# Kernel tuning notes

Measured on AMD Instinct MI355X. Metric: run time of the kernel, lower is better.

The kernel has to match this reference:

```python
import jax, jax.numpy as jnp
import numpy as np

SOFTCAP = 30.0
N_CHUNKS = 9
IGNORE_INDEX = -100


def setup_inputs() -> dict:
    key = jax.random.key(0)
    k1, k2, k3 = jax.random.split(key, 3)
    N, D, V = 576, 1024, 262400
    x = jax.random.normal(k1, (N, D), dtype=jnp.float32)
    weight = jax.random.normal(k2, (V, D), dtype=jnp.float32) * (D ** -0.5)
    labels = jax.random.randint(k3, (N,), 0, V, dtype=jnp.int64)
    return {"x": x, "weight": weight, "labels": labels}


def reference(x, weight, labels):
    """Chunked large-vocab softmax cross-entropy with tanh logit soft-capping.

    logits = SOFTCAP * tanh(x @ W.T / SOFTCAP)
    loss   = mean over valid tokens of (logsumexp(logits) - logits[label])
    Chunked over N (9 chunks) so the full [N, V] logits tensor is never
    materialized at once (mirrors the original chunked implementation).
    """
    N, D = x.shape
    chunk = N // N_CHUNKS  # N chosen divisible by N_CHUNKS
    xs = x.reshape(N_CHUNKS, chunk, D)
    ys = labels.reshape(N_CHUNKS, chunk)

    def chunk_nll_sum(xc, yc):
        # [chunk, V] logits for this chunk only
        z = SOFTCAP * jnp.tanh((xc @ weight.T) / SOFTCAP)
        lse = jax.nn.logsumexp(z, axis=-1)                       # [chunk]
        tgt = jnp.take_along_axis(z, jnp.maximum(yc, 0)[:, None], axis=1)[:, 0]
        nll = jnp.where(yc != IGNORE_INDEX, lse - tgt, 0.0)
        return jnp.sum(nll)

    def body(carry, xy):
        xc, yc = xy
        return carry + chunk_nll_sum(xc, yc), None

    total, _ = jax.lax.scan(body, jnp.float32(0.0), (xs, ys))
    n_valid = jnp.sum(labels != IGNORE_INDEX).astype(jnp.float32)
    return total / n_valid
```

## Files before the change

### kernel.cpp

```cpp
#include <hip/hip_runtime.h>
#include <hip/hip_bf16.h>

#define N_TOK   576
#define MPAD    640
#define DIM     1024
#define VOCAB   262400
#define BM      128
#define BN      128
#define BK      64
#define RB      5
#define VBLKS   (VOCAB/BN)
#define NWG     (RB*VBLKS)
#define IGNORE_INDEX (-100)

typedef float f32x4 __attribute__((ext_vector_type(4)));

#define AS1 __attribute__((address_space(1)))
#define AS3 __attribute__((address_space(3)))

__device__ __forceinline__ int cvt4_fp8(float4 v) {
  int r = __builtin_amdgcn_cvt_pk_fp8_f32(v.x, v.y, 0, false);
  r     = __builtin_amdgcn_cvt_pk_fp8_f32(v.z, v.w, r, true);
  return r;
}

__global__ void k_cvt_x(const float* __restrict__ x, unsigned char* __restrict__ xq) {
  int idx = blockIdx.x * 256 + threadIdx.x;
  long e0 = (long)idx * 8;
  int row = (int)(e0 >> 10);
  uint2 o;
  if (row < N_TOK) {
    float4 a = *(const float4*)(x + e0);
    float4 b = *(const float4*)(x + e0 + 4);
    o.x = (unsigned)cvt4_fp8(a);
    o.y = (unsigned)cvt4_fp8(b);
  } else { o.x = o.y = 0u; }
  *(uint2*)(xq + e0) = o;
}

__global__ __launch_bounds__(256, 4) void k_gemm(
    const float* __restrict__ W,
    const unsigned char* __restrict__ Xq,
    float* __restrict__ S)
{
  __shared__ unsigned char Asl[BM * BK];
  __shared__ unsigned char Bsl[BN * BK];

  const int q  = NWG / 8, rm = NWG % 8;
  const int orig = blockIdx.x;
  const int xcd  = orig & 7;
  const int part = orig >> 3;
  const int bid  = (xcd < rm ? xcd * (q + 1) : rm * (q + 1) + (xcd - rm) * q) + part;

  const int rb  = bid % RB;
  const int vb  = bid / RB;
  const int m0  = rb * BM;
  const long n0 = (long)vb * BN;

  const int t   = threadIdx.x;
  const int l   = t & 63;
  const int w   = t >> 6;
  const int wm  = w >> 1, wn = w & 1;
  const int l15 = l & 15, lh = l >> 4;

  const unsigned char* asrc[2];
  #pragma unroll
  for (int i = 0; i < 2; ++i) {
    int lin = t + i * 256;
    int p   = lin >> 3;
    int c   = (lin & 7) ^ (p & 7);
    asrc[i] = Xq + (size_t)(m0 + 2 * p + (c >> 2)) * DIM + (c & 3) * 16;
  }
  const float* bsrc[4];
  int boff[4];
  #pragma unroll
  for (int i = 0; i < 4; ++i) {
    int lin = t + i * 256;
    int r   = lin >> 3;
    int ko  = (lin & 7) * 8;
    bsrc[i] = W + (n0 + r) * DIM + ko;
    int p = r >> 1, s = r & 1;
    int jj = (lin & 7) >> 1, hb = lin & 1;
    boff[i] = p * 128 + ((((s << 2) | jj) ^ (p & 7)) << 4) + (hb << 3);
  }
  const int pr = l15 >> 1, sr = l15 & 1;
  int fo[2];
  #pragma unroll
  for (int kk = 0; kk < 2; ++kk)
    fo[kk] = pr * 128 + (((((sr << 2) | (kk * 2 + (lh >> 1))) ^ pr)) << 4)
           + ((lh & 1) << 3);
  const int abase = wm * 4096;
  const int bbase = wn * 4096;

  f32x4 acc[4][4];
  const f32x4 zero4 = {0.0f, 0.0f, 0.0f, 0.0f};
  #pragma unroll
  for (int i = 0; i < 4; ++i)
    #pragma unroll
    for (int j = 0; j < 4; ++j) acc[i][j] = zero4;

  for (int k0 = 0; k0 < DIM; k0 += BK) {
    float4 fb[4][2];
    #pragma unroll
    for (int i = 0; i < 4; ++i) {
      fb[i][0] = *(const float4*)(bsrc[i] + k0);
      fb[i][1] = *(const float4*)(bsrc[i] + k0 + 4);
    }
    __syncthreads();
    #pragma unroll
    for (int i = 0; i < 2; ++i)
      __builtin_amdgcn_global_load_lds((const AS1 void*)(asrc[i] + k0),
          (AS3 void*)(Asl + (t + i * 256) * 16), 16, 0, 0);
    #pragma unroll
    for (int i = 0; i < 4; ++i) {
      int lo = cvt4_fp8(fb[i][0]);
      int hi = cvt4_fp8(fb[i][1]);
      *(int2*)(Bsl + boff[i]) = make_int2(lo, hi);
    }
    __syncthreads();

    long af[4][2], bf[4][2];
    #pragma unroll
    for (int mi = 0; mi < 4; ++mi) {
      af[mi][0] = *(const long*)(Asl + abase + mi * 1024 + fo[0]);
      af[mi][1] = *(const long*)(Asl + abase + mi * 1024 + fo[1]);
    }
    #pragma unroll
    for (int ni = 0; ni < 4; ++ni) {
      bf[ni][0] = *(const long*)(Bsl + bbase + ni * 1024 + fo[0]);
      bf[ni][1] = *(const long*)(Bsl + bbase + ni * 1024 + fo[1]);
    }
    __builtin_amdgcn_s_setprio(1);
    #pragma unroll
    for (int kk = 0; kk < 2; ++kk)
      #pragma unroll
      for (int mi = 0; mi < 4; ++mi)
        #pragma unroll
        for (int ni = 0; ni < 4; ++ni)
          acc[mi][ni] = __builtin_amdgcn_mfma_f32_16x16x32_fp8_fp8(
              af[mi][kk], bf[ni][kk], acc[mi][ni], 0, 0, 0);
    __builtin_amdgcn_s_setprio(0);
  }

  #pragma unroll
  for (int mi = 0; mi < 4; ++mi) {
    #pragma unroll
    for (int j = 0; j < 4; ++j) {
      float s = 0.0f;
      #pragma unroll
      for (int ni = 0; ni < 4; ++ni) {
        float g   = acc[mi][ni][j];
        float tp1 = __expf(g * (1.0f / 15.0f)) + 1.0f;
        s += __expf(-60.0f * __builtin_amdgcn_rcpf(tp1));
      }
      s += __shfl_xor(s, 1);
      s += __shfl_xor(s, 2);
      s += __shfl_xor(s, 4);
      s += __shfl_xor(s, 8);
      if (l15 == 0) {
        int row = m0 + wm * 64 + mi * 16 + lh * 4 + j;
        atomicAdd(&S[row], s);
      }
    }
  }
}

__global__ void k_tgt(const float* __restrict__ x, const float* __restrict__ W,
                      const int* __restrict__ labels, float* __restrict__ tgt) {
  int n = blockIdx.x;
  int lab = labels[n];
  int t = threadIdx.x;
  float s = 0.0f;
  if (lab >= 0) {
    const float4 a = ((const float4*)(x + (size_t)n * DIM))[t];
    const float4 b = ((const float4*)(W + (size_t)lab * DIM))[t];
    s = a.x*b.x + a.y*b.y + a.z*b.z + a.w*b.w;
  }
  #pragma unroll
  for (int off = 32; off >= 1; off >>= 1) s += __shfl_xor(s, off);
  __shared__ float wsum[4];
  if ((t & 63) == 0) wsum[t >> 6] = s;
  __syncthreads();
  if (t == 0) {
    float d = wsum[0] + wsum[1] + wsum[2] + wsum[3];
    tgt[n] = (lab >= 0) ? 30.0f * tanhf(d * (1.0f / 30.0f)) : 0.0f;
  }
}

__global__ void k_final(const float* __restrict__ S, const float* __restrict__ tgt,
                        const int* __restrict__ labels, float* __restrict__ out) {
  int t = threadIdx.x;
  float sum = 0.0f, cnt = 0.0f;
  for (int n = t; n < N_TOK; n += 256) {
    if (labels[n] != IGNORE_INDEX) {
      sum += 30.0f + __logf(S[n]) - tgt[n];
      cnt += 1.0f;
    }
  }
  #pragma unroll
  for (int off = 32; off >= 1; off >>= 1) {
    sum += __shfl_xor(sum, off);
    cnt += __shfl_xor(cnt, off);
  }
  __shared__ float as_[4], ac_[4];
  if ((t & 63) == 0) { as_[t >> 6] = sum; ac_[t >> 6] = cnt; }
  __syncthreads();
  if (t == 0) out[0] = (as_[0]+as_[1]+as_[2]+as_[3]) / (ac_[0]+ac_[1]+ac_[2]+ac_[3]);
}

extern "C" void kernel_launch(void* const* d_in, const int* in_sizes, int n_in,
                              void* d_out, int out_size, void* d_ws, size_t ws_size,
                              hipStream_t stream) {
  const float* x      = (const float*)d_in[0];
  const float* W      = (const float*)d_in[1];
  const int*   labels = (const int*)d_in[2];
  float* out = (float*)d_out;

  char* ws = (char*)d_ws;
  unsigned char* xq = (unsigned char*)ws;
  float* S   = (float*)(ws + (size_t)MPAD * DIM);
  float* tgt = S + MPAD;

  hipMemsetAsync(S, 0, MPAD * sizeof(float), stream);
  k_cvt_x<<<MPAD * DIM / (256 * 8), 256, 0, stream>>>(x, xq);
  k_gemm<<<NWG, 256, 0, stream>>>(W, xq, S);
  k_tgt<<<N_TOK, 256, 0, stream>>>(x, W, labels, tgt);
  k_final<<<1, 256, 0, stream>>>(S, tgt, labels, out);
}
```

Baseline: 484.4 us.

## Load X fragments directly to registers and use 16-byte LDS reads for W

Removes the LDS staging buffer for the quantized X tile, so each wave loads its own X fragments from global memory straight into registers. It changes the k-slot assignment so each lane holds 16 contiguous bytes, which lets the W tile be read from LDS with one 16-byte load per fragment instead of two 8-byte loads. Barriers now wait only on LDS counters, which lets the global loads overlap the barrier. In exchange the X data is loaded redundantly across waves (the two waves that share wm both fetch it), register pressure rises, and launch bounds drop from 4 to 3 waves per SIMD.

```diff
diff --git a/kernel.cpp b/kernel.cpp
--- a/kernel.cpp
+++ b/kernel.cpp
@@ -15,14 +15,22 @@
 
 typedef float f32x4 __attribute__((ext_vector_type(4)));
 
-#define AS1 __attribute__((address_space(1)))
-#define AS3 __attribute__((address_space(3)))
-
 __device__ __forceinline__ int cvt4_fp8(float4 v) {
   int r = __builtin_amdgcn_cvt_pk_fp8_f32(v.x, v.y, 0, false);
   r     = __builtin_amdgcn_cvt_pk_fp8_f32(v.z, v.w, r, true);
   return r;
 }
+__device__ __forceinline__ long lo64(uint4 v) {
+  union { uint2 u; long l; } c; c.u = make_uint2(v.x, v.y); return c.l;
+}
+__device__ __forceinline__ long hi64(uint4 v) {
+  union { uint2 u; long l; } c; c.u = make_uint2(v.z, v.w); return c.l;
+}
+
+#define BARRIER() do {                                          \
+    asm volatile("s_waitcnt lgkmcnt(0)" ::: "memory");          \
+    __builtin_amdgcn_s_barrier();                               \
+  } while (0)
 
 __global__ void k_cvt_x(const float* __restrict__ x, unsigned char* __restrict__ xq) {
   int idx = blockIdx.x * 256 + threadIdx.x;
@@ -38,12 +46,11 @@
   *(uint2*)(xq + e0) = o;
 }
 
-__global__ __launch_bounds__(256, 4) void k_gemm(
+__global__ __launch_bounds__(256, 3) void k_gemm(
     const float* __restrict__ W,
     const unsigned char* __restrict__ Xq,
     float* __restrict__ S)
 {
-  __shared__ unsigned char Asl[BM * BK];
   __shared__ unsigned char Bsl[BN * BK];
 
   const int q  = NWG / 8, rm = NWG % 8;
@@ -63,34 +70,30 @@
   const int wm  = w >> 1, wn = w & 1;
   const int l15 = l & 15, lh = l >> 4;
 
-  const unsigned char* asrc[2];
-  #pragma unroll
-  for (int i = 0; i < 2; ++i) {
-    int lin = t + i * 256;
-    int p   = lin >> 3;
-    int c   = (lin & 7) ^ (p & 7);
-    asrc[i] = Xq + (size_t)(m0 + 2 * p + (c >> 2)) * DIM + (c & 3) * 16;
-  }
+  const unsigned char* asrc[4];
+  #pragma unroll
+  for (int mi = 0; mi < 4; ++mi)
+    asrc[mi] = Xq + (size_t)(m0 + wm * 64 + mi * 16 + l15) * DIM + lh * 16;
+
   const float* bsrc[4];
   int boff[4];
   #pragma unroll
   for (int i = 0; i < 4; ++i) {
     int lin = t + i * 256;
     int r   = lin >> 3;
-    int ko  = (lin & 7) * 8;
-    bsrc[i] = W + (n0 + r) * DIM + ko;
+    int g   = lin & 7;
+    bsrc[i] = W + (n0 + r) * DIM + g * 8;
     int p = r >> 1, s = r & 1;
-    int jj = (lin & 7) >> 1, hb = lin & 1;
+    int jj = g >> 1, hb = g & 1;
     boff[i] = p * 128 + ((((s << 2) | jj) ^ (p & 7)) << 4) + (hb << 3);
   }
-  const int pr = l15 >> 1, sr = l15 & 1;
-  int fo[2];
-  #pragma unroll
-  for (int kk = 0; kk < 2; ++kk)
-    fo[kk] = pr * 128 + (((((sr << 2) | (kk * 2 + (lh >> 1))) ^ pr)) << 4)
-           + ((lh & 1) << 3);
-  const int abase = wm * 4096;
-  const int bbase = wn * 4096;
+  int bro[4];
+  #pragma unroll
+  for (int ni = 0; ni < 4; ++ni) {
+    int row = wn * 64 + ni * 16 + l15;
+    int p   = row >> 1;
+    bro[ni] = p * 128 + (((((row & 1) << 2) | lh) ^ (p & 7)) << 4);
+  }
 
   f32x4 acc[4][4];
   const f32x4 zero4 = {0.0f, 0.0f, 0.0f, 0.0f};
@@ -106,39 +109,39 @@
       fb[i][0] = *(const float4*)(bsrc[i] + k0);
       fb[i][1] = *(const float4*)(bsrc[i] + k0 + 4);
     }
-    __syncthreads();
-    #pragma unroll
-    for (int i = 0; i < 2; ++i)
-      __builtin_amdgcn_global_load_lds((const AS1 void*)(asrc[i] + k0),
-          (AS3 void*)(Asl + (t + i * 256) * 16), 16, 0, 0);
+    uint4 ua[4];
+    #pragma unroll
+    for (int mi = 0; mi < 4; ++mi)
+      ua[mi] = *(const uint4*)(asrc[mi] + k0);
+
+    BARRIER();
+
     #pragma unroll
     for (int i = 0; i < 4; ++i) {
       int lo = cvt4_fp8(fb[i][0]);
       int hi = cvt4_fp8(fb[i][1]);
       *(int2*)(Bsl + boff[i]) = make_int2(lo, hi);
     }
-    __syncthreads();
-
-    long af[4][2], bf[4][2];
-    #pragma unroll
-    for (int mi = 0; mi < 4; ++mi) {
-      af[mi][0] = *(const long*)(Asl + abase + mi * 1024 + fo[0]);
-      af[mi][1] = *(const long*)(Asl + abase + mi * 1024 + fo[1]);
-    }
-    #pragma unroll
-    for (int ni = 0; ni < 4; ++ni) {
-      bf[ni][0] = *(const long*)(Bsl + bbase + ni * 1024 + fo[0]);
-      bf[ni][1] = *(const long*)(Bsl + bbase + ni * 1024 + fo[1]);
-    }
+    BARRIER();
+
+    uint4 ub[4];
+    #pragma unroll
+    for (int ni = 0; ni < 4; ++ni)
+      ub[ni] = *(const uint4*)(Bsl + bro[ni]);
+
     __builtin_amdgcn_s_setprio(1);
     #pragma unroll
-    for (int kk = 0; kk < 2; ++kk)
+    for (int mi = 0; mi < 4; ++mi)
       #pragma unroll
-      for (int mi = 0; mi < 4; ++mi)
-        #pragma unroll
-        for (int ni = 0; ni < 4; ++ni)
-          acc[mi][ni] = __builtin_amdgcn_mfma_f32_16x16x32_fp8_fp8(
-              af[mi][kk], bf[ni][kk], acc[mi][ni], 0, 0, 0);
+      for (int ni = 0; ni < 4; ++ni)
+        acc[mi][ni] = __builtin_amdgcn_mfma_f32_16x16x32_fp8_fp8(
+            lo64(ua[mi]), lo64(ub[ni]), acc[mi][ni], 0, 0, 0);
+    #pragma unroll
+    for (int mi = 0; mi < 4; ++mi)
+      #pragma unroll
+      for (int ni = 0; ni < 4; ++ni)
+        acc[mi][ni] = __builtin_amdgcn_mfma_f32_16x16x32_fp8_fp8(
+            hi64(ua[mi]), hi64(ub[ni]), acc[mi][ni], 0, 0, 0);
     __builtin_amdgcn_s_setprio(0);
   }
 
```

Measured after the change: 585.7 us. +20.9%, slower.

## Software-pipeline GEMM k-loop with double-buffered A tile and register-prefetched W

Applied to the files above, without the earlier changes.

Restructures the GEMM main loop so the next k-tile's fp8 activation tile is loaded asynchronously into a second LDS buffer, and the next W fp32 values are prefetched into registers while the current tile is computed. Explicit waitcnt and barrier placement replaces __syncthreads to overlap global loads with MFMA work. The loop is fully unrolled and launch bounds drop from 4 to 3 waves per SIMD, allowing more registers at the cost of occupancy. LDS use grows with the doubled A buffer.

```diff
diff --git a/kernel.cpp b/kernel.cpp
--- a/kernel.cpp
+++ b/kernel.cpp
@@ -8,6 +8,7 @@
 #define BM      128
 #define BN      128
 #define BK      64
+#define NT      (DIM/BK)
 #define RB      5
 #define VBLKS   (VOCAB/BN)
 #define NWG     (RB*VBLKS)
@@ -38,12 +39,12 @@
   *(uint2*)(xq + e0) = o;
 }
 
-__global__ __launch_bounds__(256, 4) void k_gemm(
+__global__ __launch_bounds__(256, 3) void k_gemm(
     const float* __restrict__ W,
     const unsigned char* __restrict__ Xq,
     float* __restrict__ S)
 {
-  __shared__ unsigned char Asl[BM * BK];
+  __shared__ unsigned char Asl[2 * BM * BK];
   __shared__ unsigned char Bsl[BN * BK];
 
   const int q  = NWG / 8, rm = NWG % 8;
@@ -77,10 +78,10 @@
   for (int i = 0; i < 4; ++i) {
     int lin = t + i * 256;
     int r   = lin >> 3;
-    int ko  = (lin & 7) * 8;
-    bsrc[i] = W + (n0 + r) * DIM + ko;
+    int g   = lin & 7;
+    bsrc[i] = W + (n0 + r) * DIM + g * 8;
     int p = r >> 1, s = r & 1;
-    int jj = (lin & 7) >> 1, hb = lin & 1;
+    int jj = g >> 1, hb = g & 1;
     boff[i] = p * 128 + ((((s << 2) | jj) ^ (p & 7)) << 4) + (hb << 3);
   }
   const int pr = l15 >> 1, sr = l15 & 1;
@@ -99,31 +100,58 @@
     #pragma unroll
     for (int j = 0; j < 4; ++j) acc[i][j] = zero4;
 
-  for (int k0 = 0; k0 < DIM; k0 += BK) {
-    float4 fb[4][2];
-    #pragma unroll
-    for (int i = 0; i < 4; ++i) {
-      fb[i][0] = *(const float4*)(bsrc[i] + k0);
-      fb[i][1] = *(const float4*)(bsrc[i] + k0 + 4);
-    }
-    __syncthreads();
-    #pragma unroll
-    for (int i = 0; i < 2; ++i)
-      __builtin_amdgcn_global_load_lds((const AS1 void*)(asrc[i] + k0),
-          (AS3 void*)(Asl + (t + i * 256) * 16), 16, 0, 0);
+  float4 fb[4][2];
+
+  #pragma unroll
+  for (int i = 0; i < 2; ++i)
+    __builtin_amdgcn_global_load_lds((const AS1 void*)(asrc[i]),
+        (AS3 void*)(Asl + (t + i * 256) * 16), 16, 0, 0);
+  #pragma unroll
+  for (int i = 0; i < 4; ++i) {
+    fb[i][0] = *(const float4*)(bsrc[i]);
+    fb[i][1] = *(const float4*)(bsrc[i] + 4);
+  }
+
+  #pragma unroll
+  for (int kt = 0; kt < NT; ++kt) {
+    const int rbuf = kt & 1;
+
+    asm volatile("s_waitcnt lgkmcnt(0)" ::: "memory");
+    __builtin_amdgcn_s_barrier();
+    __builtin_amdgcn_sched_barrier(0);
+
+    if (kt < NT - 1) {
+      #pragma unroll
+      for (int i = 0; i < 2; ++i)
+        __builtin_amdgcn_global_load_lds(
+            (const AS1 void*)(asrc[i] + (kt + 1) * BK),
+            (AS3 void*)(Asl + (rbuf ^ 1) * 8192 + (t + i * 256) * 16), 16, 0, 0);
+    }
     #pragma unroll
     for (int i = 0; i < 4; ++i) {
       int lo = cvt4_fp8(fb[i][0]);
       int hi = cvt4_fp8(fb[i][1]);
       *(int2*)(Bsl + boff[i]) = make_int2(lo, hi);
     }
-    __syncthreads();
+    if (kt < NT - 1) {
+      #pragma unroll
+      for (int i = 0; i < 4; ++i) {
+        fb[i][0] = *(const float4*)(bsrc[i] + (kt + 1) * BK);
+        fb[i][1] = *(const float4*)(bsrc[i] + (kt + 1) * BK + 4);
+      }
+    }
+    asm volatile("s_waitcnt lgkmcnt(0)" ::: "memory");
+    if (kt < NT - 1) asm volatile("s_waitcnt vmcnt(10)" ::: "memory");
+    else             asm volatile("s_waitcnt vmcnt(0)"  ::: "memory");
+    __builtin_amdgcn_sched_barrier(0);
+    __builtin_amdgcn_s_barrier();
+    __builtin_amdgcn_sched_barrier(0);
 
     long af[4][2], bf[4][2];
     #pragma unroll
     for (int mi = 0; mi < 4; ++mi) {
-      af[mi][0] = *(const long*)(Asl + abase + mi * 1024 + fo[0]);
-      af[mi][1] = *(const long*)(Asl + abase + mi * 1024 + fo[1]);
+      af[mi][0] = *(const long*)(Asl + rbuf * 8192 + abase + mi * 1024 + fo[0]);
+      af[mi][1] = *(const long*)(Asl + rbuf * 8192 + abase + mi * 1024 + fo[1]);
     }
     #pragma unroll
     for (int ni = 0; ni < 4; ++ni) {
```

New measurement: 497.1 us. +2.6%, slower.

## Fuse x-cast and target kernels; load A tile via registers with new LDS swizzle

Applied to the files above, without the earlier changes.

Merges the x fp8 conversion and target-logit kernels into one prep launch, which removes a kernel launch and its gap. In the GEMM, the A tile is now loaded through registers into a redesigned 8-byte-granularity swizzled LDS layout instead of using global_load_lds. The plain __syncthreads is replaced by an explicit lgkmcnt wait, barrier and sched_barrier, which lets the global loads for A and B be issued before the first barrier. The trade is extra VGPR pressure and more LDS store instructions per thread, with the risk that the new swizzle brings different bank conflicts.

```diff
diff --git a/kernel.cpp b/kernel.cpp
--- a/kernel.cpp
+++ b/kernel.cpp
@@ -15,27 +15,53 @@
 
 typedef float f32x4 __attribute__((ext_vector_type(4)));
 
-#define AS1 __attribute__((address_space(1)))
-#define AS3 __attribute__((address_space(3)))
-
 __device__ __forceinline__ int cvt4_fp8(float4 v) {
   int r = __builtin_amdgcn_cvt_pk_fp8_f32(v.x, v.y, 0, false);
   r     = __builtin_amdgcn_cvt_pk_fp8_f32(v.z, v.w, r, true);
   return r;
 }
 
-__global__ void k_cvt_x(const float* __restrict__ x, unsigned char* __restrict__ xq) {
-  int idx = blockIdx.x * 256 + threadIdx.x;
-  long e0 = (long)idx * 8;
-  int row = (int)(e0 >> 10);
-  uint2 o;
-  if (row < N_TOK) {
-    float4 a = *(const float4*)(x + e0);
-    float4 b = *(const float4*)(x + e0 + 4);
-    o.x = (unsigned)cvt4_fp8(a);
-    o.y = (unsigned)cvt4_fp8(b);
-  } else { o.x = o.y = 0u; }
-  *(uint2*)(xq + e0) = o;
+#define BARRIER() do {                                          \
+    asm volatile("s_waitcnt lgkmcnt(0)" ::: "memory");          \
+    __builtin_amdgcn_s_barrier();                               \
+    __builtin_amdgcn_sched_barrier(0);                          \
+  } while (0)
+
+__global__ void k_prep(const float* __restrict__ x, const float* __restrict__ W,
+                       const int* __restrict__ labels,
+                       unsigned char* __restrict__ xq, float* __restrict__ tgt) {
+  if (blockIdx.x < MPAD * DIM / 2048) {
+    int idx = blockIdx.x * 256 + threadIdx.x;
+    long e0 = (long)idx * 8;
+    int row = (int)(e0 >> 10);
+    uint2 o;
+    if (row < N_TOK) {
+      float4 a = *(const float4*)(x + e0);
+      float4 b = *(const float4*)(x + e0 + 4);
+      o.x = (unsigned)cvt4_fp8(a);
+      o.y = (unsigned)cvt4_fp8(b);
+    } else { o.x = o.y = 0u; }
+    *(uint2*)(xq + e0) = o;
+  } else {
+    int n = blockIdx.x - MPAD * DIM / 2048;
+    int lab = labels[n];
+    int t = threadIdx.x;
+    float s = 0.0f;
+    if (lab >= 0) {
+      const float4 a = ((const float4*)(x + (size_t)n * DIM))[t];
+      const float4 b = ((const float4*)(W + (size_t)lab * DIM))[t];
+      s = a.x*b.x + a.y*b.y + a.z*b.z + a.w*b.w;
+    }
+    #pragma unroll
+    for (int off = 32; off >= 1; off >>= 1) s += __shfl_xor(s, off);
+    __shared__ float wsum[4];
+    if ((t & 63) == 0) wsum[t >> 6] = s;
+    __syncthreads();
+    if (t == 0) {
+      float d = wsum[0] + wsum[1] + wsum[2] + wsum[3];
+      tgt[n] = (lab >= 0) ? 30.0f * tanhf(d * (1.0f / 30.0f)) : 0.0f;
+    }
+  }
 }
 
 __global__ __launch_bounds__(256, 4) void k_gemm(
@@ -64,12 +90,16 @@
   const int l15 = l & 15, lh = l >> 4;
 
   const unsigned char* asrc[2];
+  int aoff0[2], aoff1[2];
   #pragma unroll
   for (int i = 0; i < 2; ++i) {
     int lin = t + i * 256;
-    int p   = lin >> 3;
-    int c   = (lin & 7) ^ (p & 7);
-    asrc[i] = Xq + (size_t)(m0 + 2 * p + (c >> 2)) * DIM + (c & 3) * 16;
+    int r   = lin >> 2;
+    int c16 = lin & 3;
+    asrc[i] = Xq + (size_t)(m0 + r) * DIM + c16 * 16;
+    int p = r >> 1, s = r & 1, pp = p & 7;
+    aoff0[i] = p * 128 + (s * 8 + ((2 * c16)     ^ pp)) * 8;
+    aoff1[i] = p * 128 + (s * 8 + ((2 * c16 + 1) ^ pp)) * 8;
   }
   const float* bsrc[4];
   int boff[4];
@@ -77,18 +107,16 @@
   for (int i = 0; i < 4; ++i) {
     int lin = t + i * 256;
     int r   = lin >> 3;
-    int ko  = (lin & 7) * 8;
-    bsrc[i] = W + (n0 + r) * DIM + ko;
+    int k8  = lin & 7;
+    bsrc[i] = W + (n0 + r) * DIM + k8 * 8;
     int p = r >> 1, s = r & 1;
-    int jj = (lin & 7) >> 1, hb = lin & 1;
-    boff[i] = p * 128 + ((((s << 2) | jj) ^ (p & 7)) << 4) + (hb << 3);
+    boff[i] = p * 128 + (s * 8 + (k8 ^ (p & 7))) * 8;
   }
   const int pr = l15 >> 1, sr = l15 & 1;
   int fo[2];
   #pragma unroll
   for (int kk = 0; kk < 2; ++kk)
-    fo[kk] = pr * 128 + (((((sr << 2) | (kk * 2 + (lh >> 1))) ^ pr)) << 4)
-           + ((lh & 1) << 3);
+    fo[kk] = pr * 128 + sr * 64 + (((kk * 4 + lh) ^ pr)) * 8;
   const int abase = wm * 4096;
   const int bbase = wn * 4096;
 
@@ -106,18 +134,25 @@
       fb[i][0] = *(const float4*)(bsrc[i] + k0);
       fb[i][1] = *(const float4*)(bsrc[i] + k0 + 4);
     }
-    __syncthreads();
+    uint4 ua[2];
     #pragma unroll
     for (int i = 0; i < 2; ++i)
-      __builtin_amdgcn_global_load_lds((const AS1 void*)(asrc[i] + k0),
-          (AS3 void*)(Asl + (t + i * 256) * 16), 16, 0, 0);
+      ua[i] = *(const uint4*)(asrc[i] + k0);
+
+    BARRIER();
+
+    #pragma unroll
+    for (int i = 0; i < 2; ++i) {
+      *(uint2*)(Asl + aoff0[i]) = make_uint2(ua[i].x, ua[i].y);
+      *(uint2*)(Asl + aoff1[i]) = make_uint2(ua[i].z, ua[i].w);
+    }
     #pragma unroll
     for (int i = 0; i < 4; ++i) {
       int lo = cvt4_fp8(fb[i][0]);
       int hi = cvt4_fp8(fb[i][1]);
       *(int2*)(Bsl + boff[i]) = make_int2(lo, hi);
     }
-    __syncthreads();
+    BARRIER();
 
     long af[4][2], bf[4][2];
     #pragma unroll
@@ -165,28 +200,6 @@
   }
 }
 
-__global__ void k_tgt(const float* __restrict__ x, const float* __restrict__ W,
-                      const int* __restrict__ labels, float* __restrict__ tgt) {
-  int n = blockIdx.x;
-  int lab = labels[n];
-  int t = threadIdx.x;
-  float s = 0.0f;
-  if (lab >= 0) {
-    const float4 a = ((const float4*)(x + (size_t)n * DIM))[t];
-    const float4 b = ((const float4*)(W + (size_t)lab * DIM))[t];
-    s = a.x*b.x + a.y*b.y + a.z*b.z + a.w*b.w;
-  }
-  #pragma unroll
-  for (int off = 32; off >= 1; off >>= 1) s += __shfl_xor(s, off);
-  __shared__ float wsum[4];
-  if ((t & 63) == 0) wsum[t >> 6] = s;
-  __syncthreads();
-  if (t == 0) {
-    float d = wsum[0] + wsum[1] + wsum[2] + wsum[3];
-    tgt[n] = (lab >= 0) ? 30.0f * tanhf(d * (1.0f / 30.0f)) : 0.0f;
-  }
-}
-
 __global__ void k_final(const float* __restrict__ S, const float* __restrict__ tgt,
                         const int* __restrict__ labels, float* __restrict__ out) {
   int t = threadIdx.x;
@@ -222,8 +235,7 @@
   float* tgt = S + MPAD;
 
   hipMemsetAsync(S, 0, MPAD * sizeof(float), stream);
-  k_cvt_x<<<MPAD * DIM / (256 * 8), 256, 0, stream>>>(x, xq);
+  k_prep<<<MPAD * DIM / 2048 + N_TOK, 256, 0, stream>>>(x, W, labels, xq, tgt);
   k_gemm<<<NWG, 256, 0, stream>>>(W, xq, S);
-  k_tgt<<<N_TOK, 256, 0, stream>>>(x, W, labels, tgt);
   k_final<<<1, 256, 0, stream>>>(S, tgt, labels, out);
 }
```

After: 551.2 us. 1.14x slower.
